# Optimization experiments

Hardware: AMD Instinct MI355X
Metric: run time of the kernel (lower is better)

## Reference

```python
import jax, jax.numpy as jnp
import numpy as np

N_QUBITS = 8
N_LAYERS = 3
DIM = 2 ** N_QUBITS  # 256


def _ry(t):
    # t: scalar or [B] -> [2,2] or [B,2,2] complex64
    c = jnp.cos(t / 2).astype(jnp.complex64)
    s = jnp.sin(t / 2).astype(jnp.complex64)
    return jnp.stack([jnp.stack([c, -s], -1), jnp.stack([s, c], -1)], -2)


def _rz(t):
    e = jnp.exp(-0.5j * t.astype(jnp.complex64))
    z = jnp.zeros_like(e)
    return jnp.stack([jnp.stack([e, z], -1), jnp.stack([z, jnp.conj(e)], -1)], -2)


def _rx(t):
    c = jnp.cos(t / 2).astype(jnp.complex64)
    s = (-1j) * jnp.sin(t / 2).astype(jnp.complex64)
    return jnp.stack([jnp.stack([c, s], -1), jnp.stack([s, c], -1)], -2)


def _apply_1q(state, U, wire):
    # state: [B, 256] complex64; U: [2,2] (shared) or [B,2,2] (per-sample)
    B = state.shape[0]
    l = 2 ** wire
    r = 2 ** (N_QUBITS - wire - 1)
    s = state.reshape(B, l, 2, r)
    if U.ndim == 2:
        s = jnp.einsum('ij,bljr->blir', U, s)
    else:
        s = jnp.einsum('bij,bljr->blir', U, s)
    return s.reshape(B, DIM)


def _apply_cnot(state, c_wire):
    # CNOT with control c_wire, target c_wire+1 (adjacent, as in the circuit)
    B = state.shape[0]
    l = 2 ** c_wire
    r = 2 ** (N_QUBITS - c_wire - 2)
    s = state.reshape(B, l, 2, 2, r)  # [B, left, ctrl, tgt, right]
    s = jnp.stack([s[:, :, 0], s[:, :, 1, ::-1]], axis=2)  # flip target where ctrl=1
    return s.reshape(B, DIM)


def _circuit(x, weights):
    B = x.shape[0]
    state = jnp.zeros((B, DIM), jnp.complex64).at[:, 0].set(1.0)
    # angle encoding: RY(x_i*pi) then RZ(x_i*pi) on each wire (per-sample angles)
    for i in range(N_QUBITS):
        ang = x[:, i] * jnp.pi
        state = _apply_1q(state, _ry(ang), i)
        state = _apply_1q(state, _rz(ang), i)
    # variational layers: RX(w), RY(w) per qubit, then CNOT ladder
    idx = 0
    for _ in range(N_LAYERS):
        for q in range(N_QUBITS):
            state = _apply_1q(state, _rx(weights[idx]), q)
            state = _apply_1q(state, _ry(weights[idx + 1]), q)
            idx += 2
        for q in range(N_QUBITS - 1):
            state = _apply_cnot(state, q)
    # <Z_i> = P(bit_i = 0) - P(bit_i = 1)
    p = (jnp.abs(state) ** 2).reshape((B,) + (2,) * N_QUBITS)
    outs = []
    for i in range(N_QUBITS):
        axes = tuple(j + 1 for j in range(N_QUBITS) if j != i)
        m = p.sum(axes)  # [B, 2]
        outs.append(m[:, 0] - m[:, 1])
    return jnp.stack(outs, -1).astype(jnp.float32)  # [B, 8]


def setup_inputs() -> dict:
    key = jax.random.key(0)
    k1, k2 = jax.random.split(key)
    x = jax.random.normal(k1, (16384, 8), dtype=jnp.float32)
    weights = jax.random.normal(k2, (48,), dtype=jnp.float32) * 0.1
    return {"x": x, "weights": weights}


def reference(x, weights):
    return _circuit(x, weights)
```

## Files before the change

### kernel.cpp

```cpp
#include <hip/hip_runtime.h>
#include <math.h>

#define PI_F 3.14159265358979323846f

typedef _Float16 h16x8 __attribute__((ext_vector_type(8)));
typedef float f32x4 __attribute__((ext_vector_type(4)));
typedef unsigned int u32x4 __attribute__((ext_vector_type(4)));

#define APAGE 4112


__device__ __forceinline__ void gpair(float2& a, const float2 p, const int mb,
                                      const float g0x, const float g0y,
                                      const float g1x, const float g1y) {
    const float e0y = mb ? -g0y : g0y;
    const float f1x = mb ? -g1x : g1x;
    const float nx = g0x * a.x - e0y * a.y + f1x * p.x - g1y * p.y;
    const float ny = g0x * a.y + e0y * a.x + f1x * p.y + g1y * p.x;
    a.x = nx; a.y = ny;
}

__device__ __forceinline__ void apply_g(float2 a[4], const int b, const int lane,
                                        const float g0x, const float g0y,
                                        const float g1x, const float g1y) {
    if (b >= 2) {
        const int lb = b - 2;
        const int mb = (lane >> lb) & 1;
#pragma unroll
        for (int j = 0; j < 4; ++j) {
            float2 p;
            p.x = __shfl_xor(a[j].x, 1 << lb, 64);
            p.y = __shfl_xor(a[j].y, 1 << lb, 64);
            gpair(a[j], p, mb, g0x, g0y, g1x, g1y);
        }
    } else if (b == 1) {
        float2 o0 = a[0], o1 = a[1], o2 = a[2], o3 = a[3];
        gpair(a[0], o2, 0, g0x, g0y, g1x, g1y);
        gpair(a[2], o0, 1, g0x, g0y, g1x, g1y);
        gpair(a[1], o3, 0, g0x, g0y, g1x, g1y);
        gpair(a[3], o1, 1, g0x, g0y, g1x, g1y);
    } else {
        float2 o0 = a[0], o1 = a[1], o2 = a[2], o3 = a[3];
        gpair(a[0], o1, 0, g0x, g0y, g1x, g1y);
        gpair(a[1], o0, 1, g0x, g0y, g1x, g1y);
        gpair(a[2], o3, 0, g0x, g0y, g1x, g1y);
        gpair(a[3], o2, 1, g0x, g0y, g1x, g1y);
    }
}

__device__ __forceinline__ void apply_cnot_g(float2 a[4], const int cw, const int lane) {
    if (cw <= 4) {
        const int lt = (6 - cw) - 2;
        const int lc = lt + 1;
        const bool ctrl = ((lane >> lc) & 1) != 0;
#pragma unroll
        for (int j = 0; j < 4; ++j) {
            float px = __shfl_xor(a[j].x, 1 << lt, 64);
            float py = __shfl_xor(a[j].y, 1 << lt, 64);
            a[j].x = ctrl ? px : a[j].x;
            a[j].y = ctrl ? py : a[j].y;
        }
    } else if (cw == 5) {
        const bool ctrl = (lane & 1) != 0;
        float2 t;
        t = a[0]; a[0].x = ctrl ? a[2].x : a[0].x; a[0].y = ctrl ? a[2].y : a[0].y;
        a[2].x = ctrl ? t.x : a[2].x; a[2].y = ctrl ? t.y : a[2].y;
        t = a[1]; a[1].x = ctrl ? a[3].x : a[1].x; a[1].y = ctrl ? a[3].y : a[1].y;
        a[3].x = ctrl ? t.x : a[3].x; a[3].y = ctrl ? t.y : a[3].y;
    } else {
        float2 t = a[2]; a[2] = a[3]; a[3] = t;
    }
}

__device__ __forceinline__ unsigned int packh2(float lo, float hi) {
    unsigned short l = __builtin_bit_cast(unsigned short, (_Float16)lo);
    unsigned short h = __builtin_bit_cast(unsigned short, (_Float16)hi);
    return ((unsigned int)h << 16) | (unsigned int)l;
}

__device__ __forceinline__ float2 cmulf(float2 a, float2 b) {
    return make_float2(a.x * b.x - a.y * b.y, a.x * b.y + a.y * b.x);
}

__device__ __forceinline__ h16x8 negh8(h16x8 v) {
    u32x4 u = __builtin_bit_cast(u32x4, v);
    u ^= (u32x4){0x80008000u, 0x80008000u, 0x80008000u, 0x80008000u};
    return __builtin_bit_cast(h16x8, u);
}

__global__ __launch_bounds__(64) void ubuild_kernel(const float* __restrict__ w,
                                                    unsigned short* __restrict__ ub16) {
    __shared__ float wc[48];
    __shared__ float wsn[48];
    const int tid = threadIdx.x;
    if (tid < 48) {
        float s, c;
        __sincosf(w[tid] * 0.5f, &s, &c);
        wc[tid] = c; wsn[tid] = s;
    }
    __syncthreads();

    const int lane = tid;
    const int n = blockIdx.x;

    float2 a[4];
#pragma unroll
    for (int j = 0; j < 4; ++j) {
        a[j].x = (lane * 4 + j == n) ? 1.0f : 0.0f;
        a[j].y = 0.0f;
    }

#pragma unroll
    for (int L = 0; L < 3; ++L) {
#pragma unroll
        for (int q = 0; q < 8; ++q) {
            const int k = 2 * (L * 8 + q);
            const float c0 = wc[k], s0 = wsn[k];
            const float c1 = wc[k + 1], s1 = wsn[k + 1];
            const float g0x = c1 * c0, g0y = s1 * s0;
            const float g1x = -s1 * c0, g1y = -c1 * s0;
            apply_g(a, 7 - q, lane, g0x, g0y, g1x, g1y);
        }
#pragma unroll
        for (int cwire = 0; cwire < 7; ++cwire) apply_cnot_g(a, cwire, lane);
    }

    const int base = (n >> 5) * 8192 + (n & 31);
#pragma unroll
    for (int j = 0; j < 4; ++j) {
        const int m = lane * 4 + j;
        ub16[base + m * 32] =
            __builtin_bit_cast(unsigned short, (_Float16)a[j].x);
        ub16[65536 + base + m * 32] =
            __builtin_bit_cast(unsigned short, (_Float16)a[j].y);
    }
}

__device__ __forceinline__ void loadB4(h16x8 bf[4], const char* ub, const size_t boff[4],
                                       const int kk) {
#pragma unroll
    for (int f = 0; f < 4; ++f)
        bf[f] = *(const h16x8*)(ub + (size_t)kk * 16384 + boff[f]);
}

__device__ __forceinline__ void loadA8(h16x8 ar[4], h16x8 ai[4], const char* apc,
                                       const unsigned int aoff, const int kk) {
#pragma unroll
    for (int rt = 0; rt < 4; ++rt)
        ar[rt] = *(const h16x8*)(apc + kk * APAGE + rt * 1024 + aoff);
#pragma unroll
    for (int rt = 0; rt < 4; ++rt)
        ai[rt] = *(const h16x8*)(apc + 8 * APAGE + kk * APAGE + rt * 1024 + aoff);
}

__device__ __forceinline__ void mfma32(f32x4 aR[4][2], f32x4 aI[4][2],
                                       const h16x8 ar[4], const h16x8 ai[4],
                                       const h16x8 bf[4]) {
#pragma unroll
    for (int rt = 0; rt < 4; ++rt) {
        const h16x8 nai = negh8(ai[rt]);
#pragma unroll
        for (int cf = 0; cf < 2; ++cf) {
            aR[rt][cf] = __builtin_amdgcn_mfma_f32_16x16x32_f16(ar[rt], bf[cf],
                                                                aR[rt][cf], 0, 0, 0);
            aR[rt][cf] = __builtin_amdgcn_mfma_f32_16x16x32_f16(nai, bf[2 + cf],
                                                                aR[rt][cf], 0, 0, 0);
            aI[rt][cf] = __builtin_amdgcn_mfma_f32_16x16x32_f16(ai[rt], bf[cf],
                                                                aI[rt][cf], 0, 0, 0);
            aI[rt][cf] = __builtin_amdgcn_mfma_f32_16x16x32_f16(ar[rt], bf[2 + cf],
                                                                aI[rt][cf], 0, 0, 0);
        }
    }
}

__global__ __launch_bounds__(512, 2) void gemm_kernel(const float* __restrict__ x,
                                                      const unsigned short* __restrict__ upack,
                                                      float* __restrict__ out) {
    __shared__ char Ap[16 * APAGE];
    __shared__ float zbuf[8][64][8];

    const int tid = threadIdx.x;

    {
        const int row = tid >> 3;
        const int t8 = tid & 7;
        const int grow = blockIdx.x * 64 + row;

        const float4* xp = (const float4*)(x + grow * 8);
        float4 xa = xp[0], xb = xp[1];
        float ang[8] = {xa.x, xa.y, xa.z, xa.w, xb.x, xb.y, xb.z, xb.w};

        float2 v0[8], v1[8];
#pragma unroll
        for (int i = 0; i < 8; ++i) {
            float s, c;
            __sincosf(ang[i] * (PI_F * 0.5f), &s, &c);
            v0[i] = make_float2(c * c, -c * s);
            v1[i] = make_float2(s * c, s * s);
        }

        float2 pre = (t8 & 4) ? v1[0] : v0[0];
        pre = cmulf(pre, (t8 & 2) ? v1[1] : v0[1]);
        pre = cmulf(pre, (t8 & 1) ? v1[2] : v0[2]);

        const int swz = (row >> 1) & 3;
        char* reb = Ap + t8 * APAGE + row * 64;
        char* imb = Ap + (8 + t8) * APAGE + row * 64;

#pragma unroll
        for (int b4 = 0; b4 < 2; ++b4) {
            float2 p3 = cmulf(pre, b4 ? v1[3] : v0[3]);
#pragma unroll
            for (int b3 = 0; b3 < 2; ++b3) {
                float2 p4 = cmulf(p3, b3 ? v1[4] : v0[4]);
                u32x4 qre, qim;
#pragma unroll
                for (int b2 = 0; b2 < 2; ++b2) {
                    float2 p5 = cmulf(p4, b2 ? v1[5] : v0[5]);
#pragma unroll
                    for (int b1 = 0; b1 < 2; ++b1) {
                        float2 p6 = cmulf(p5, b1 ? v1[6] : v0[6]);
                        const float2 amp0 = cmulf(p6, v0[7]);
                        const float2 amp1 = cmulf(p6, v1[7]);
                        const int pos = (b2 << 1) | b1;
                        qre[pos] = packh2(amp0.x, amp1.x);
                        qim[pos] = packh2(amp0.y, amp1.y);
                    }
                }
                const int c = (b4 << 1) | b3;
                *(u32x4*)(reb + ((c ^ swz) * 16)) = qre;
                *(u32x4*)(imb + ((c ^ swz) * 16)) = qim;
            }
        }
    }
    __syncthreads();

    const int lane = tid & 63;
    const int wv = tid >> 6;
    const int c15 = lane & 15;
    const int g = lane >> 4;

    const char* ub = (const char*)upack;
    size_t boff[4];
    {
        const int cb0 = wv * 32;
        boff[0] = (size_t)(cb0 + c15) * 64 + g * 16;
        boff[1] = (size_t)(cb0 + 16 + c15) * 64 + g * 16;
        boff[2] = 131072 + boff[0];
        boff[3] = 131072 + boff[1];
    }
    const unsigned int aoff = c15 * 64 + ((g ^ ((c15 >> 1) & 3)) * 16);
    const char* apc = (const char*)Ap;

    f32x4 aR[4][2], aI[4][2];
#pragma unroll
    for (int rt = 0; rt < 4; ++rt)
#pragma unroll
        for (int cf = 0; cf < 2; ++cf) {
            f32x4 z = {0.f, 0.f, 0.f, 0.f};
            aR[rt][cf] = z; aI[rt][cf] = z;
        }

    h16x8 b0[4], b1[4], b2[4], b3[4];
    h16x8 ar0[4], ai0[4], ar1[4], ai1[4];

    loadB4(b0, ub, boff, 0);
    loadB4(b1, ub, boff, 1);
    loadB4(b2, ub, boff, 2);
    loadB4(b3, ub, boff, 3);
    loadA8(ar0, ai0, apc, aoff, 0);

    loadA8(ar1, ai1, apc, aoff, 1);  mfma32(aR, aI, ar0, ai0, b0);  loadB4(b0, ub, boff, 4);
    loadA8(ar0, ai0, apc, aoff, 2);  mfma32(aR, aI, ar1, ai1, b1);  loadB4(b1, ub, boff, 5);
    loadA8(ar1, ai1, apc, aoff, 3);  mfma32(aR, aI, ar0, ai0, b2);  loadB4(b2, ub, boff, 6);
    loadA8(ar0, ai0, apc, aoff, 4);  mfma32(aR, aI, ar1, ai1, b3);  loadB4(b3, ub, boff, 7);
    loadA8(ar1, ai1, apc, aoff, 5);  mfma32(aR, aI, ar0, ai0, b0);
    loadA8(ar0, ai0, apc, aoff, 6);  mfma32(aR, aI, ar1, ai1, b1);
    loadA8(ar1, ai1, apc, aoff, 7);  mfma32(aR, aI, ar0, ai0, b2);
                                     mfma32(aR, aI, ar1, ai1, b3);

    const float sg0 = (wv & 4) ? -1.f : 1.f;
    const float sg1 = (wv & 2) ? -1.f : 1.f;
    const float sg2 = (wv & 1) ? -1.f : 1.f;

#pragma unroll
    for (int rt = 0; rt < 4; ++rt) {
#pragma unroll
        for (int r = 0; r < 4; ++r) {
            const float p0 = aR[rt][0][r] * aR[rt][0][r] + aI[rt][0][r] * aI[rt][0][r];
            const float p1 = aR[rt][1][r] * aR[rt][1][r] + aI[rt][1][r] * aI[rt][1][r];
            float S = p0 + p1;
            float Sd = p0 - p1;
#pragma unroll
            for (int b = 0; b < 4; ++b) {
                float u = __shfl_xor(S, 1 << b, 64);
                S = ((c15 >> b) & 1) ? (u - S) : (S + u);
            }
#pragma unroll
            for (int b = 0; b < 4; ++b) Sd += __shfl_xor(Sd, 1 << b, 64);

            const int rowl = rt * 16 + g * 4 + r;
            if (c15 == 0) {
                zbuf[wv][rowl][0] = sg0 * S;
                zbuf[wv][rowl][1] = sg1 * S;
                zbuf[wv][rowl][2] = sg2 * S;
                zbuf[wv][rowl][3] = Sd;
            } else if (c15 == 8) {
                zbuf[wv][rowl][4] = S;
            } else if (c15 == 4) {
                zbuf[wv][rowl][5] = S;
            } else if (c15 == 2) {
                zbuf[wv][rowl][6] = S;
            } else if (c15 == 1) {
                zbuf[wv][rowl][7] = S;
            }
        }
    }
    __syncthreads();

    {
        const int row = tid >> 3;
        const int i = tid & 7;
        float v = 0.f;
#pragma unroll
        for (int w2 = 0; w2 < 8; ++w2) v += zbuf[w2][row][i];
        out[(blockIdx.x * 64 + row) * 8 + i] = v;
    }
}

extern "C" void kernel_launch(void* const* d_in, const int* in_sizes, int n_in,
                              void* d_out, int out_size, void* d_ws, size_t ws_size,
                              hipStream_t stream) {
    const float* x = (const float*)d_in[0];
    const float* w = (const float*)d_in[1];
    float* out = (float*)d_out;
    const int B = in_sizes[0] / 8;

    unsigned short* ub16 = (unsigned short*)d_ws;
    ubuild_kernel<<<256, 64, 0, stream>>>(w, ub16);

    gemm_kernel<<<B / 64, 512, 0, stream>>>(x, (const unsigned short*)d_ws, out);
}
```

Measured before the change: 24.57 us.

## Analytic first layer in unitary build, early B loads, restructured Z reduction

The unitary-build kernel now computes the first variational layer analytically as a product state (using a Gray-code index for the CNOT ladder) rather than simulating it gate by gate. In the GEMM kernel, the B-fragment global loads move ahead of the state-encoding phase so their latency overlaps with the sincos and LDS writes. The epilogue replaces per-row shuffle butterflies and branchy zbuf writes with LDS staging of probability pairs. A per-thread Walsh-style reduction then follows, finishing with a short shuffle and vectorized output stores. This adds an extra barrier and reuses the A LDS region, and the early loads raise register pressure.

Result: faster. 20.49 us (-16.6%).

```diff
diff --git a/kernel.cpp b/kernel.cpp
--- a/kernel.cpp
+++ b/kernel.cpp
@@ -8,6 +8,7 @@
 typedef unsigned int u32x4 __attribute__((ext_vector_type(4)));
 
 #define APAGE 4112
+#define P2STR 146
 
 
 __device__ __forceinline__ void gpair(float2& a, const float2 p, const int mb,
@@ -103,15 +104,34 @@
     const int lane = tid;
     const int n = blockIdx.x;
 
+    float2 e0q[8], e1q[8];
+#pragma unroll
+    for (int q = 0; q < 8; ++q) {
+        const int k = 2 * q;
+        const float c0 = wc[k], s0 = wsn[k];
+        const float c1 = wc[k + 1], s1 = wsn[k + 1];
+        const float2 g0 = make_float2(c1 * c0, s1 * s0);
+        const float2 g1 = make_float2(-s1 * c0, -c1 * s0);
+        const int nq = (n >> (7 - q)) & 1;
+        e0q[q] = nq ? g1 : g0;
+        e1q[q] = nq ? make_float2(g0.x, -g0.y)
+                    : make_float2(-g1.x, g1.y);
+    }
+
     float2 a[4];
 #pragma unroll
     for (int j = 0; j < 4; ++j) {
-        a[j].x = (lane * 4 + j == n) ? 1.0f : 0.0f;
-        a[j].y = 0.0f;
-    }
-
-#pragma unroll
-    for (int L = 0; L < 3; ++L) {
+        const int m = lane * 4 + j;
+        const int v = m ^ (m >> 1);
+        float2 acc = ((v >> 7) & 1) ? e1q[0] : e0q[0];
+#pragma unroll
+        for (int q = 1; q < 8; ++q)
+            acc = cmulf(acc, ((v >> (7 - q)) & 1) ? e1q[q] : e0q[q]);
+        a[j] = acc;
+    }
+
+#pragma unroll
+    for (int L = 1; L < 3; ++L) {
 #pragma unroll
         for (int q = 0; q < 8; ++q) {
             const int k = 2 * (L * 8 + q);
@@ -176,10 +196,28 @@
 __global__ __launch_bounds__(512, 2) void gemm_kernel(const float* __restrict__ x,
                                                       const unsigned short* __restrict__ upack,
                                                       float* __restrict__ out) {
-    __shared__ char Ap[16 * APAGE];
-    __shared__ float zbuf[8][64][8];
+    __shared__ __align__(16) char smem[64 * P2STR * 8];
 
     const int tid = threadIdx.x;
+    const int lane = tid & 63;
+    const int wv = tid >> 6;
+    const int c15 = lane & 15;
+    const int g = lane >> 4;
+
+    const char* ub = (const char*)upack;
+    size_t boff[4];
+    {
+        const int cb0 = wv * 32;
+        boff[0] = (size_t)(cb0 + c15) * 64 + g * 16;
+        boff[1] = (size_t)(cb0 + 16 + c15) * 64 + g * 16;
+        boff[2] = 131072 + boff[0];
+        boff[3] = 131072 + boff[1];
+    }
+    h16x8 b0[4], b1[4], b2[4], b3[4];
+    loadB4(b0, ub, boff, 0);
+    loadB4(b1, ub, boff, 1);
+    loadB4(b2, ub, boff, 2);
+    loadB4(b3, ub, boff, 3);
 
     {
         const int row = tid >> 3;
@@ -204,8 +242,8 @@
         pre = cmulf(pre, (t8 & 1) ? v1[2] : v0[2]);
 
         const int swz = (row >> 1) & 3;
-        char* reb = Ap + t8 * APAGE + row * 64;
-        char* imb = Ap + (8 + t8) * APAGE + row * 64;
+        char* reb = smem + t8 * APAGE + row * 64;
+        char* imb = smem + (8 + t8) * APAGE + row * 64;
 
 #pragma unroll
         for (int b4 = 0; b4 < 2; ++b4) {
@@ -235,22 +273,8 @@
     }
     __syncthreads();
 
-    const int lane = tid & 63;
-    const int wv = tid >> 6;
-    const int c15 = lane & 15;
-    const int g = lane >> 4;
-
-    const char* ub = (const char*)upack;
-    size_t boff[4];
-    {
-        const int cb0 = wv * 32;
-        boff[0] = (size_t)(cb0 + c15) * 64 + g * 16;
-        boff[1] = (size_t)(cb0 + 16 + c15) * 64 + g * 16;
-        boff[2] = 131072 + boff[0];
-        boff[3] = 131072 + boff[1];
-    }
     const unsigned int aoff = c15 * 64 + ((g ^ ((c15 >> 1) & 3)) * 16);
-    const char* apc = (const char*)Ap;
+    const char* apc = (const char*)smem;
 
     f32x4 aR[4][2], aI[4][2];
 #pragma unroll
@@ -261,13 +285,7 @@
             aR[rt][cf] = z; aI[rt][cf] = z;
         }
 
-    h16x8 b0[4], b1[4], b2[4], b3[4];
     h16x8 ar0[4], ai0[4], ar1[4], ai1[4];
-
-    loadB4(b0, ub, boff, 0);
-    loadB4(b1, ub, boff, 1);
-    loadB4(b2, ub, boff, 2);
-    loadB4(b3, ub, boff, 3);
     loadA8(ar0, ai0, apc, aoff, 0);
 
     loadA8(ar1, ai1, apc, aoff, 1);  mfma32(aR, aI, ar0, ai0, b0);  loadB4(b0, ub, boff, 4);
@@ -279,52 +297,73 @@
     loadA8(ar1, ai1, apc, aoff, 7);  mfma32(aR, aI, ar0, ai0, b2);
                                      mfma32(aR, aI, ar1, ai1, b3);
 
-    const float sg0 = (wv & 4) ? -1.f : 1.f;
-    const float sg1 = (wv & 2) ? -1.f : 1.f;
-    const float sg2 = (wv & 1) ? -1.f : 1.f;
-
-#pragma unroll
-    for (int rt = 0; rt < 4; ++rt) {
-#pragma unroll
-        for (int r = 0; r < 4; ++r) {
-            const float p0 = aR[rt][0][r] * aR[rt][0][r] + aI[rt][0][r] * aI[rt][0][r];
-            const float p1 = aR[rt][1][r] * aR[rt][1][r] + aI[rt][1][r] * aI[rt][1][r];
-            float S = p0 + p1;
-            float Sd = p0 - p1;
-#pragma unroll
-            for (int b = 0; b < 4; ++b) {
-                float u = __shfl_xor(S, 1 << b, 64);
-                S = ((c15 >> b) & 1) ? (u - S) : (S + u);
+    __syncthreads();
+
+    {
+        float2* P2 = (float2*)smem;
+#pragma unroll
+        for (int rt = 0; rt < 4; ++rt) {
+#pragma unroll
+            for (int r = 0; r < 4; ++r) {
+                const float p0 = aR[rt][0][r] * aR[rt][0][r] + aI[rt][0][r] * aI[rt][0][r];
+                const float p1 = aR[rt][1][r] * aR[rt][1][r] + aI[rt][1][r] * aI[rt][1][r];
+                const int row = rt * 16 + g * 4 + r;
+                P2[row * P2STR + wv * 18 + c15] = make_float2(p0, p1);
             }
-#pragma unroll
-            for (int b = 0; b < 4; ++b) Sd += __shfl_xor(Sd, 1 << b, 64);
-
-            const int rowl = rt * 16 + g * 4 + r;
-            if (c15 == 0) {
-                zbuf[wv][rowl][0] = sg0 * S;
-                zbuf[wv][rowl][1] = sg1 * S;
-                zbuf[wv][rowl][2] = sg2 * S;
-                zbuf[wv][rowl][3] = Sd;
-            } else if (c15 == 8) {
-                zbuf[wv][rowl][4] = S;
-            } else if (c15 == 4) {
-                zbuf[wv][rowl][5] = S;
-            } else if (c15 == 2) {
-                zbuf[wv][rowl][6] = S;
-            } else if (c15 == 1) {
-                zbuf[wv][rowl][7] = S;
-            }
         }
     }
     __syncthreads();
 
     {
+        const float2* P2 = (const float2*)smem;
         const int row = tid >> 3;
-        const int i = tid & 7;
-        float v = 0.f;
-#pragma unroll
-        for (int w2 = 0; w2 < 8; ++w2) v += zbuf[w2][row][i];
-        out[(blockIdx.x * 64 + row) * 8 + i] = v;
+        const int w2 = tid & 7;
+
+        const float4* base = (const float4*)(P2 + row * P2STR + w2 * 18);
+        float S[16], D[16];
+#pragma unroll
+        for (int k = 0; k < 8; ++k) {
+            const float4 q = base[k];
+            S[2 * k]     = q.x + q.y;  D[2 * k]     = q.x - q.y;
+            S[2 * k + 1] = q.z + q.w;  D[2 * k + 1] = q.z - q.w;
+        }
+        float s2[8], w1p[8];
+#pragma unroll
+        for (int k = 0; k < 8; ++k) { s2[k] = S[2*k] + S[2*k+1]; w1p[k] = S[2*k] - S[2*k+1]; }
+        float s4[4], w2p[4];
+#pragma unroll
+        for (int k = 0; k < 4; ++k) { s4[k] = s2[2*k] + s2[2*k+1]; w2p[k] = s2[2*k] - s2[2*k+1]; }
+        const float s8a = s4[0] + s4[1], s8b = s4[2] + s4[3];
+        const float W0 = s8a + s8b;
+        const float W8 = s8a - s8b;
+        const float W4 = (s4[0] - s4[1]) + (s4[2] - s4[3]);
+        const float W2 = w2p[0] + w2p[1] + w2p[2] + w2p[3];
+        float W1 = 0.f, Sd = 0.f;
+#pragma unroll
+        for (int k = 0; k < 8; ++k) { W1 += w1p[k]; Sd += D[2*k] + D[2*k+1]; }
+
+        float zp[8];
+        zp[0] = (w2 & 4) ? -W0 : W0;
+        zp[1] = (w2 & 2) ? -W0 : W0;
+        zp[2] = (w2 & 1) ? -W0 : W0;
+        zp[3] = Sd;
+        zp[4] = W8;
+        zp[5] = W4;
+        zp[6] = W2;
+        zp[7] = W1;
+
+#pragma unroll
+        for (int i = 0; i < 8; ++i) {
+            zp[i] += __shfl_xor(zp[i], 1, 64);
+            zp[i] += __shfl_xor(zp[i], 2, 64);
+            zp[i] += __shfl_xor(zp[i], 4, 64);
+        }
+
+        if (w2 == 0) {
+            float* po = out + (size_t)(blockIdx.x * 64 + row) * 8;
+            *(float4*)po       = make_float4(zp[0], zp[1], zp[2], zp[3]);
+            *(float4*)(po + 4) = make_float4(zp[4], zp[5], zp[6], zp[7]);
+        }
     }
 }
 
```
